# Kernel tuning notes

Hardware: AMD Instinct MI355X
Metric: run time of the kernel (lower is better)

The kernel has to match this reference:

```python
import jax, jax.numpy as jnp
import numpy as np

N = 100000      # num nodes
E = 1600000     # num edges
IN = 128        # in_channels
OUT = 128       # out_channels
K = 2           # num_k_hops


def setup_inputs() -> dict:
    key = jax.random.key(0)
    k1, k2, k3 = jax.random.split(key, 3)
    x = jax.random.normal(k1, (N, IN), dtype=jnp.float32)
    edge_index = jax.random.randint(k2, (2, E), 0, N, dtype=jnp.int32)
    # Linear(in, out) params, kaiming-uniform-ish scale
    W = jax.random.normal(k3, (OUT, IN), dtype=jnp.float32) * (1.0 / np.sqrt(IN))
    b = jnp.zeros((OUT,), dtype=jnp.float32)
    return {"x": x, "edge_index": edge_index, "W": W, "b": b}


def reference(x, edge_index, W, b):
    n = x.shape[0]
    # gcn_norm: add self-loops, symmetric normalization deg^-1/2 A_hat deg^-1/2
    loop = jnp.arange(n, dtype=edge_index.dtype)
    row = jnp.concatenate([edge_index[0], loop])  # source j
    col = jnp.concatenate([edge_index[1], loop])  # target i
    deg = jax.ops.segment_sum(jnp.ones_like(col, dtype=x.dtype), col, num_segments=n)
    dinv = jnp.where(deg > 0, jax.lax.rsqrt(deg), jnp.zeros_like(deg))
    norm = dinv[row] * dinv[col]  # [E+N]

    def hop(h, _):
        # out[i] = sum_{(j->i)} norm_ij * h[j]  (gather + scatter-add SpMM)
        msg = norm[:, None] * h[row]
        return jax.ops.segment_sum(msg, col, num_segments=n), None

    h, _ = jax.lax.scan(hop, x, None, length=K)
    # final linear projection (SGConv.lin)
    return h @ W.T + b
```

## Files before the change

kernel.cpp:

```cpp
#include <hip/hip_runtime.h>

#define CAP 64
#define NPB 256
#define NPB_SHIFT 8
#define CAPB 4864
#define EPB 4096
#define MAXB 512
#define BBT 1024

typedef __attribute__((ext_vector_type(8))) _Float16 half8v;
typedef __attribute__((ext_vector_type(2))) _Float16 h2v;
typedef __attribute__((ext_vector_type(4))) float f32x4;

__device__ __forceinline__ unsigned pkh2(float x, float y) {
  h2v h;
  h[0] = (_Float16)x;
  h[1] = (_Float16)y;
  return __builtin_bit_cast(unsigned, h);
}

__global__ __launch_bounds__(256) void k_binA(const int* __restrict__ row,
                                              const int* __restrict__ col,
                                              int* __restrict__ gcur,
                                              unsigned int* __restrict__ binned,
                                              int E, int nb) {
  __shared__ int lcnt[MAXB];
  int tid = threadIdx.x;
  for (int i = tid; i < nb; i += 256) lcnt[i] = 0;
  __syncthreads();
  int e0 = blockIdx.x * EPB;
#pragma unroll
  for (int it = 0; it < EPB / 256; ++it) {
    int e = e0 + it * 256 + tid;
    if (e < E) atomicAdd(&lcnt[col[e] >> NPB_SHIFT], 1);
  }
  __syncthreads();
  for (int b = tid; b < nb; b += 256) {
    int c = lcnt[b];
    lcnt[b] = (c > 0) ? atomicAdd(&gcur[b], c) : 0;
  }
  __syncthreads();
#pragma unroll
  for (int it = 0; it < EPB / 256; ++it) {
    int e = e0 + it * 256 + tid;
    if (e < E) {
      int c = col[e];
      int s = row[e];
      int b = c >> NPB_SHIFT;
      int pos = atomicAdd(&lcnt[b], 1);
      if (pos < (b + 1) * CAPB)
        binned[pos] = ((unsigned)s << NPB_SHIFT) | (unsigned)(c & (NPB - 1));
    }
  }
}

__global__ __launch_bounds__(BBT) void k_binB(const unsigned int* __restrict__ binned,
                                              const int* __restrict__ gcur,
                                              int* __restrict__ counts,
                                              float* __restrict__ dinv,
                                              int* __restrict__ srcbuf,
                                              const float2* __restrict__ x2,
                                              unsigned* __restrict__ xh,
                                              int N) {
  __shared__ int cur[NPB];
  __shared__ float dl[NPB];
  int tid = threadIdx.x;
  int b = blockIdx.x;
  if (tid < NPB) cur[tid] = 0;
  __syncthreads();
  int cnt = gcur[b] - b * CAPB;
  if (cnt > CAPB) cnt = CAPB;
  const unsigned int* bp = binned + (size_t)b * CAPB;
  int nb0 = b << NPB_SHIFT;
  int e = tid;
  for (; e + 3 * BBT < cnt; e += 4 * BBT) {
    unsigned p0 = bp[e];
    unsigned p1 = bp[e + BBT];
    unsigned p2 = bp[e + 2 * BBT];
    unsigned p3 = bp[e + 3 * BBT];
    int r0 = atomicAdd(&cur[p0 & (NPB - 1)], 1);
    if (r0 < CAP - 1) srcbuf[((size_t)(nb0 + (p0 & (NPB - 1))) << 6) + r0] = (int)(p0 >> NPB_SHIFT);
    int r1 = atomicAdd(&cur[p1 & (NPB - 1)], 1);
    if (r1 < CAP - 1) srcbuf[((size_t)(nb0 + (p1 & (NPB - 1))) << 6) + r1] = (int)(p1 >> NPB_SHIFT);
    int r2 = atomicAdd(&cur[p2 & (NPB - 1)], 1);
    if (r2 < CAP - 1) srcbuf[((size_t)(nb0 + (p2 & (NPB - 1))) << 6) + r2] = (int)(p2 >> NPB_SHIFT);
    int r3 = atomicAdd(&cur[p3 & (NPB - 1)], 1);
    if (r3 < CAP - 1) srcbuf[((size_t)(nb0 + (p3 & (NPB - 1))) << 6) + r3] = (int)(p3 >> NPB_SHIFT);
  }
  for (; e < cnt; e += BBT) {
    unsigned p = bp[e];
    int li = p & (NPB - 1);
    int r = atomicAdd(&cur[li], 1);
    if (r < CAP - 1) srcbuf[((size_t)(nb0 + li) << 6) + r] = (int)(p >> NPB_SHIFT);
  }
  __syncthreads();
  if (tid < NPB) {
    int node = nb0 + tid;
    if (node < N) {
      int c = cur[tid];
      int mlen = (c < CAP - 1) ? c : (CAP - 1);
      int* myp = srcbuf + ((size_t)node << 6);
      myp[mlen] = node;
      int cntp = (mlen + 1 + 7) & ~7;
      for (int p2 = mlen + 1; p2 < cntp; ++p2) myp[p2] = N;
      counts[node] = cntp;
      float d = rsqrtf((float)c + 1.0f);
      dinv[node] = d;
      dl[tid] = d;
    }
  }
  __syncthreads();
#pragma unroll
  for (int it = 0; it < 8; ++it) {
    int idx0 = (it * 2) * BBT + tid;
    int idx1 = (it * 2 + 1) * BBT + tid;
    float2 v0, v1;
    bool ok0 = nb0 + (idx0 >> 6) < N;
    bool ok1 = nb0 + (idx1 >> 6) < N;
    if (ok0) v0 = x2[((size_t)nb0 << 6) + idx0];
    if (ok1) v1 = x2[((size_t)nb0 << 6) + idx1];
    if (ok0) {
      float d = dl[idx0 >> 6];
      xh[((size_t)nb0 << 6) + idx0] = pkh2(v0.x * d, v0.y * d);
    }
    if (ok1) {
      float d = dl[idx1 >> 6];
      xh[((size_t)nb0 << 6) + idx1] = pkh2(v1.x * d, v1.y * d);
    }
  }
}

__global__ void k_init(int* __restrict__ gcur, int nb) {
  int i = blockIdx.x * blockDim.x + threadIdx.x;
  if (i < nb) gcur[i] = i * CAPB;
}

#define PACC(v)                                   \
  A[0] += __builtin_bit_cast(h2v, (v).x);         \
  A[1] += __builtin_bit_cast(h2v, (v).y);         \
  A[2] += __builtin_bit_cast(h2v, (v).z);         \
  A[3] += __builtin_bit_cast(h2v, (v).w);

template <int MODE>
__global__ __launch_bounds__(256) void k_hop(
    const unsigned* __restrict__ hin, unsigned* __restrict__ hout,
    const int* __restrict__ srcbuf, const int* __restrict__ counts,
    const float* __restrict__ dinv, int n) {
  int wave = __builtin_amdgcn_readfirstlane((int)(threadIdx.x >> 6));
  int lane = threadIdx.x & 63;
  int node = blockIdx.x * 4 + wave;
  if (node >= n) return;
  int cntp = counts[node];
  float di = dinv[node];
  int g = lane >> 4;
  int m = lane & 15;
  const uint4* h4 = (const uint4*)hin;
  const int* sp = srcbuf + ((size_t)node << 6);
  h2v A[4];
#pragma unroll
  for (int q = 0; q < 4; ++q) A[q] = (h2v)(_Float16)0;
  int e = 0;
  for (; e + 16 <= cntp; e += 16) {
    int s0 = sp[e + g];
    int s1 = sp[e + 4 + g];
    int s2 = sp[e + 8 + g];
    int s3 = sp[e + 12 + g];
    uint4 v0 = h4[((size_t)s0 << 4) + m];
    uint4 v1 = h4[((size_t)s1 << 4) + m];
    uint4 v2 = h4[((size_t)s2 << 4) + m];
    uint4 v3 = h4[((size_t)s3 << 4) + m];
    PACC(v0); PACC(v1); PACC(v2); PACC(v3);
  }
  if (e < cntp) {
    int s0 = sp[e + g];
    int s1 = sp[e + 4 + g];
    uint4 v0 = h4[((size_t)s0 << 4) + m];
    uint4 v1 = h4[((size_t)s1 << 4) + m];
    PACC(v0); PACC(v1);
  }
#pragma unroll
  for (int q = 0; q < 4; ++q) {
    A[q] += __builtin_bit_cast(h2v, __shfl_xor(__builtin_bit_cast(int, A[q]), 32));
    A[q] += __builtin_bit_cast(h2v, __shfl_xor(__builtin_bit_cast(int, A[q]), 16));
  }
  float s = (MODE == 1) ? di * di : di;
  if (g == 0) {
    uint4 o;
    o.x = pkh2((float)A[0][0] * s, (float)A[0][1] * s);
    o.y = pkh2((float)A[1][0] * s, (float)A[1][1] * s);
    o.z = pkh2((float)A[2][0] * s, (float)A[2][1] * s);
    o.w = pkh2((float)A[3][0] * s, (float)A[3][1] * s);
    *(uint4*)&hout[((size_t)node << 6) + (m << 2)] = o;
  }
}

__global__ __launch_bounds__(256) void k_gemm_mfma(
    const unsigned* __restrict__ h2h, const float* __restrict__ W,
    const float* __restrict__ bias, float* __restrict__ out, int n) {
  __shared__ _Float16 Wl[128 * 128];
  int tid = threadIdx.x;
  const float4* Wg4 = (const float4*)W;
#pragma unroll
  for (int it = 0; it < 8; ++it) {
    int idx = tid + (it << 8);
    int c = idx >> 4;
    int j = idx & 15;
    float4 a = Wg4[c * 32 + j * 2];
    float4 bq = Wg4[c * 32 + j * 2 + 1];
    half8v s;
    s[0] = (_Float16)a.x;  s[1] = (_Float16)a.y;
    s[2] = (_Float16)a.z;  s[3] = (_Float16)a.w;
    s[4] = (_Float16)bq.x; s[5] = (_Float16)bq.y;
    s[6] = (_Float16)bq.z; s[7] = (_Float16)bq.w;
    int eo = (j << 3) ^ ((c & 7) << 3);
    *(half8v*)&Wl[(c << 7) + eo] = s;
  }
  __syncthreads();

  int wv = __builtin_amdgcn_readfirstlane((int)(tid >> 6));
  int lane = tid & 63;
  int tiles = (n + 15) >> 4;
  int tile = blockIdx.x * 4 + wv;
  if (tile >= tiles) return;
  int row0 = tile << 4;
  int r = lane & 15, g = lane >> 4;

  int arow = row0 + r;
  if (arow >= n) arow = n - 1;
  const _Float16* hrow = (const _Float16*)(h2h + ((size_t)arow << 6));
  half8v A0 = *(const half8v*)&hrow[g * 8];
  half8v A1 = *(const half8v*)&hrow[g * 8 + 32];
  half8v A2 = *(const half8v*)&hrow[g * 8 + 64];
  half8v A3 = *(const half8v*)&hrow[g * 8 + 96];

#pragma unroll
  for (int ct = 0; ct < 8; ++ct) {
    int c = (ct << 4) + r;
    int sw = (c & 7) << 3;
    const _Float16* wrow = &Wl[c << 7];
    half8v B0 = *(const half8v*)&wrow[(g * 8) ^ sw];
    half8v B1 = *(const half8v*)&wrow[(g * 8 + 32) ^ sw];
    half8v B2 = *(const half8v*)&wrow[(g * 8 + 64) ^ sw];
    half8v B3 = *(const half8v*)&wrow[(g * 8 + 96) ^ sw];
    f32x4 acc = {0.f, 0.f, 0.f, 0.f};
    acc = __builtin_amdgcn_mfma_f32_16x16x32_f16(A0, B0, acc, 0, 0, 0);
    acc = __builtin_amdgcn_mfma_f32_16x16x32_f16(A1, B1, acc, 0, 0, 0);
    acc = __builtin_amdgcn_mfma_f32_16x16x32_f16(A2, B2, acc, 0, 0, 0);
    acc = __builtin_amdgcn_mfma_f32_16x16x32_f16(A3, B3, acc, 0, 0, 0);
    float bb = bias[c];
#pragma unroll
    for (int q = 0; q < 4; ++q) {
      int rr = row0 + g * 4 + q;
      if (rr < n) out[(size_t)rr * 128 + c] = acc[q] + bb;
    }
  }
}

extern "C" void kernel_launch(void* const* d_in, const int* in_sizes, int n_in,
                              void* d_out, int out_size, void* d_ws, size_t ws_size,
                              hipStream_t stream) {
  const float* x = (const float*)d_in[0];
  const int* ei = (const int*)d_in[1];
  const float* W = (const float*)d_in[2];
  const float* b = (const float*)d_in[3];
  int N = in_sizes[0] / 128;
  int E = in_sizes[1] / 2;
  float* out = (float*)d_out;

  char* ws = (char*)d_ws;
  int* counts = (int*)ws;
  float* dinv = (float*)(ws + (512u << 10));
  int* gcur = (int*)(ws + (960u << 10));
  int* srcbuf = (int*)(ws + (1u << 20));
  unsigned* xh = (unsigned*)(ws + (27u << 20));
  unsigned* h2h = xh;
  unsigned* h1h = (unsigned*)(ws + (53u << 20));
  unsigned int* binned = (unsigned int*)(ws + (53u << 20));

  int nb = (N + NPB - 1) >> NPB_SHIFT;
  int blocksA = (E + EPB - 1) / EPB;
  int tiles = (N + 15) >> 4;

  hipMemsetAsync(xh + ((size_t)N << 6), 0, 256, stream);
  hipMemsetAsync(h1h + ((size_t)N << 6), 0, 256, stream);

  k_init<<<(nb + 255) / 256, 256, 0, stream>>>(gcur, nb);
  k_binA<<<blocksA, 256, 0, stream>>>(ei, ei + E, gcur, binned, E, nb);
  k_binB<<<nb, BBT, 0, stream>>>(binned, gcur, counts, dinv, srcbuf,
                                 (const float2*)x, xh, N);
  k_hop<1><<<(N + 3) / 4, 256, 0, stream>>>(xh, h1h, srcbuf, counts, dinv, N);
  k_hop<2><<<(N + 3) / 4, 256, 0, stream>>>(h1h, h2h, srcbuf, counts, dinv, N);
  k_gemm_mfma<<<(tiles + 3) / 4, 256, 0, stream>>>(h2h, W, b, out, N);
}
```

Before: 199.7 us.

## Split hop SpMM into feature slices with slice-major intermediate layout

The hop kernels now split the 128 features into 8 slices of 16 halves, with each block handling one slice of a 256-node bucket. Each 16-lane group processes one node, 8 edges per step at 32 bytes per lane pair. The intermediate h1 is stored slice-major so that each slice's gathered working set is small and more likely to stay cache-resident. The cost is many more gather requests of smaller size, divergent while-loops, and a final scale done in fp16 rather than fp32.

```diff
diff --git a/kernel.cpp b/kernel.cpp
--- a/kernel.cpp
+++ b/kernel.cpp
@@ -135,62 +135,71 @@
   if (i < nb) gcur[i] = i * CAPB;
 }
 
-#define PACC(v)                                   \
-  A[0] += __builtin_bit_cast(h2v, (v).x);         \
-  A[1] += __builtin_bit_cast(h2v, (v).y);         \
-  A[2] += __builtin_bit_cast(h2v, (v).z);         \
-  A[3] += __builtin_bit_cast(h2v, (v).w);
-
 template <int MODE>
 __global__ __launch_bounds__(256) void k_hop(
     const unsigned* __restrict__ hin, unsigned* __restrict__ hout,
     const int* __restrict__ srcbuf, const int* __restrict__ counts,
     const float* __restrict__ dinv, int n) {
-  int wave = __builtin_amdgcn_readfirstlane((int)(threadIdx.x >> 6));
-  int lane = threadIdx.x & 63;
-  int node = blockIdx.x * 4 + wave;
-  if (node >= n) return;
-  int cntp = counts[node];
-  float di = dinv[node];
-  int g = lane >> 4;
-  int m = lane & 15;
-  const uint4* h4 = (const uint4*)hin;
-  const int* sp = srcbuf + ((size_t)node << 6);
-  h2v A[4];
-#pragma unroll
-  for (int q = 0; q < 4; ++q) A[q] = (h2v)(_Float16)0;
-  int e = 0;
-  for (; e + 16 <= cntp; e += 16) {
-    int s0 = sp[e + g];
-    int s1 = sp[e + 4 + g];
-    int s2 = sp[e + 8 + g];
-    int s3 = sp[e + 12 + g];
-    uint4 v0 = h4[((size_t)s0 << 4) + m];
-    uint4 v1 = h4[((size_t)s1 << 4) + m];
-    uint4 v2 = h4[((size_t)s2 << 4) + m];
-    uint4 v3 = h4[((size_t)s3 << 4) + m];
-    PACC(v0); PACC(v1); PACC(v2); PACC(v3);
-  }
-  if (e < cntp) {
-    int s0 = sp[e + g];
-    int s1 = sp[e + 4 + g];
-    uint4 v0 = h4[((size_t)s0 << 4) + m];
-    uint4 v1 = h4[((size_t)s1 << 4) + m];
-    PACC(v0); PACC(v1);
-  }
-#pragma unroll
-  for (int q = 0; q < 4; ++q) {
-    A[q] += __builtin_bit_cast(h2v, __shfl_xor(__builtin_bit_cast(int, A[q]), 32));
-    A[q] += __builtin_bit_cast(h2v, __shfl_xor(__builtin_bit_cast(int, A[q]), 16));
-  }
-  float s = (MODE == 1) ? di * di : di;
-  if (g == 0) {
-    uint4 o;
-    o.x = pkh2((float)A[0][0] * s, (float)A[0][1] * s);
-    o.y = pkh2((float)A[1][0] * s, (float)A[1][1] * s);
-    o.z = pkh2((float)A[2][0] * s, (float)A[2][1] * s);
-    o.w = pkh2((float)A[3][0] * s, (float)A[3][1] * s);
-    *(uint4*)&hout[((size_t)node << 6) + (m << 2)] = o;
+  int blk = blockIdx.x;
+  int slice = blk & 7;
+  int bucket = blk >> 3;
+  int nb0 = bucket << 8;
+  int tid = threadIdx.x;
+  int wid = tid >> 6;
+  int lane = tid & 63;
+  int grp = lane >> 4;
+  int sub = (lane >> 1) & 7;
+  int m = lane & 1;
+  const uint4* in4 = (const uint4*)hin;
+  uint4* out4 = (uint4*)hout;
+  size_t sbase = (size_t)slice * (size_t)(n + 1) * 2;
+  int so2 = slice * 2 + m;
+
+  if (MODE == 1 && bucket == 0 && tid < 2) {
+    out4[sbase + (size_t)n * 2 + tid] = make_uint4(0, 0, 0, 0);
+  }
+
+  for (int it = 0; it < 16; ++it) {
+    int node = nb0 + (wid << 6) + (it << 2) + grp;
+    bool ok = node < n;
+    int cnt = ok ? counts[node] : 0;
+    float di = ok ? dinv[node] : 1.0f;
+    const int* sp = srcbuf + ((size_t)node << 6);
+    h2v a0 = (h2v)(_Float16)0, a1 = a0, a2 = a0, a3 = a0;
+    int e = 0;
+    while (__any(e < cnt)) {
+      int x = e + sub;
+      int src = (x < cnt) ? sp[x] : n;
+      size_t ii = (MODE == 1) ? ((size_t)src * 16 + so2)
+                              : (sbase + (size_t)src * 2 + m);
+      uint4 v = in4[ii];
+      a0 += __builtin_bit_cast(h2v, v.x);
+      a1 += __builtin_bit_cast(h2v, v.y);
+      a2 += __builtin_bit_cast(h2v, v.z);
+      a3 += __builtin_bit_cast(h2v, v.w);
+      e += 8;
+    }
+#pragma unroll
+    for (int off = 2; off <= 8; off <<= 1) {
+      a0 += __builtin_bit_cast(h2v, __shfl_xor(__builtin_bit_cast(int, a0), off));
+      a1 += __builtin_bit_cast(h2v, __shfl_xor(__builtin_bit_cast(int, a1), off));
+      a2 += __builtin_bit_cast(h2v, __shfl_xor(__builtin_bit_cast(int, a2), off));
+      a3 += __builtin_bit_cast(h2v, __shfl_xor(__builtin_bit_cast(int, a3), off));
+    }
+    if ((lane & 14) == 0 && ok) {
+      _Float16 hs = (_Float16)((MODE == 1) ? di * di : di);
+      h2v hv;
+      hv[0] = hs;
+      hv[1] = hs;
+      uint4 o;
+      o.x = __builtin_bit_cast(unsigned, (h2v)(a0 * hv));
+      o.y = __builtin_bit_cast(unsigned, (h2v)(a1 * hv));
+      o.z = __builtin_bit_cast(unsigned, (h2v)(a2 * hv));
+      o.w = __builtin_bit_cast(unsigned, (h2v)(a3 * hv));
+      size_t oi = (MODE == 1) ? (sbase + (size_t)node * 2 + m)
+                              : ((size_t)node * 16 + so2);
+      out4[oi] = o;
+    }
   }
 }
 
@@ -274,7 +283,7 @@
   int* srcbuf = (int*)(ws + (1u << 20));
   unsigned* xh = (unsigned*)(ws + (27u << 20));
   unsigned* h2h = xh;
-  unsigned* h1h = (unsigned*)(ws + (53u << 20));
+  unsigned* h1s = (unsigned*)(ws + (53u << 20));
   unsigned int* binned = (unsigned int*)(ws + (53u << 20));
 
   int nb = (N + NPB - 1) >> NPB_SHIFT;
@@ -282,13 +291,12 @@
   int tiles = (N + 15) >> 4;
 
   hipMemsetAsync(xh + ((size_t)N << 6), 0, 256, stream);
-  hipMemsetAsync(h1h + ((size_t)N << 6), 0, 256, stream);
 
   k_init<<<(nb + 255) / 256, 256, 0, stream>>>(gcur, nb);
   k_binA<<<blocksA, 256, 0, stream>>>(ei, ei + E, gcur, binned, E, nb);
   k_binB<<<nb, BBT, 0, stream>>>(binned, gcur, counts, dinv, srcbuf,
                                  (const float2*)x, xh, N);
-  k_hop<1><<<(N + 3) / 4, 256, 0, stream>>>(xh, h1h, srcbuf, counts, dinv, N);
-  k_hop<2><<<(N + 3) / 4, 256, 0, stream>>>(h1h, h2h, srcbuf, counts, dinv, N);
+  k_hop<1><<<nb * 8, 256, 0, stream>>>(xh, h1s, srcbuf, counts, dinv, N);
+  k_hop<2><<<nb * 8, 256, 0, stream>>>(h1s, h2h, srcbuf, counts, dinv, N);
   k_gemm_mfma<<<(tiles + 3) / 4, 256, 0, stream>>>(h2h, W, b, out, N);
 }
```

Result: slower. 394.9 us (+97.7%).
